# Optimization experiments

Hardware: AMD Instinct MI355X
Metric: run time of the kernel (lower is better)

Reference implementation:

```python
import math
import jax, jax.numpy as jnp
import numpy as np

B, S, D = 2, 2048, 1024
H = 16
R = 256
NC = 16
NE = 16
NK = 4096
KR = 256
TOPK = 8


def setup_inputs() -> dict:
    key = jax.random.key(0)
    ks = jax.random.split(key, 16)
    n = lambda k, shape, s: jax.random.normal(k, shape, jnp.float32) * s
    d = {}
    d['x'] = jax.random.normal(ks[0], (B, S, D), jnp.float32)
    d['importance'] = jax.random.uniform(ks[1], (B, S), jnp.float32)
    # global router weights (nn.Linear(d_model, n, bias=False) -> [n, d_model])
    d['Wc'] = n(ks[2], (NC, D), 0.02)
    d['WQ'] = n(ks[3], (NE, D), 0.02)
    d['WK'] = n(ks[4], (NE, D), 0.02)
    d['WV'] = n(ks[5], (NE, D), 0.02)
    d['Wm'] = n(ks[6], (NC, D), 0.02)
    # shared neuron pools (orthogonal init approximated by scaled gaussian)
    d['compress_neurons'] = n(ks[7], (NC, D, R), 1.0 / math.sqrt(D))
    d['expand_pool'] = n(ks[8], (NE, R, D), 1.0 / math.sqrt(R))
    d['knowledge_K'] = n(ks[9], (NK, KR), 0.02)
    d['knowledge_V'] = n(ks[10], (NK, D), 0.02)
    d['W_O'] = n(ks[11], (D, D), 1.0 / math.sqrt(D))
    d['g1'] = jnp.ones((D,), jnp.float32)
    d['b1'] = jnp.zeros((D,), jnp.float32)
    d['g2'] = jnp.ones((D,), jnp.float32)
    d['b2'] = jnp.zeros((D,), jnp.float32)
    return d


def _ln(x, g, b):
    mu = x.mean(-1, keepdims=True)
    v = ((x - mu) ** 2).mean(-1, keepdims=True)
    return (x - mu) * jax.lax.rsqrt(v + 1e-5) * g + b


def _route(nx, imp, W):
    # softmax over expert axis, importance-weighted pool over sequence, renormalize
    pref = jax.nn.softmax(nx @ W.T, axis=-1)          # [B,S,n]
    w = jnp.einsum('bs,bsn->bn', imp, pref)
    return w / (w.sum(-1, keepdims=True) + 1e-8)


def reference(x, importance, Wc, WQ, WK, WV, Wm, compress_neurons, expand_pool,
              knowledge_K, knowledge_V, W_O, g1, b1, g2, b2):
    Bx, Sx, Dm = x.shape
    dh = Dm // H
    # --- attention sub-block ---
    nx = _ln(x, g1, b1)
    cw = _route(nx, importance, Wc)
    qw = _route(nx, importance, WQ)
    kw = _route(nx, importance, WK)
    vw = _route(nx, importance, WV)
    sc = jnp.einsum('bn,ndr->bdr', cw, compress_neurons)   # per-batch compress [B,D,R]
    h = jnp.einsum('bsd,bdr->bsr', nx, sc)                 # [B,S,R]

    def expand(w):
        e = jnp.einsum('bn,nrd->brd', w, expand_pool)      # [B,R,D]
        return jnp.einsum('bsr,brd->bsd', h, e)            # [B,S,D]

    Q = expand(qw).reshape(Bx, Sx, H, dh).transpose(0, 2, 1, 3)
    K = expand(kw).reshape(Bx, Sx, H, dh).transpose(0, 2, 1, 3)
    V = expand(vw).reshape(Bx, Sx, H, dh).transpose(0, 2, 1, 3)
    scores = jnp.einsum('bhqd,bhkd->bhqk', Q, K) / math.sqrt(dh)
    causal = jnp.tril(jnp.ones((Sx, Sx), bool))
    scores = jnp.where(causal, scores, -jnp.inf)
    attn = jax.nn.softmax(scores, axis=-1)
    ao = jnp.einsum('bhqk,bhkd->bhqd', attn, V)
    ao = ao.transpose(0, 2, 1, 3).reshape(Bx, Sx, Dm)
    x = x + ao @ W_O.T
    # --- memory sub-block ---
    nx2 = _ln(x, g2, b2)
    mw = _route(nx2, importance, Wm)
    mc = jnp.einsum('bn,ndr->bdr', mw, compress_neurons)
    Qm = jnp.einsum('bsd,bdr->bsr', nx2, mc)              # [B,S,R]
    ms = Qm @ knowledge_K.T / math.sqrt(KR)               # [B,S,NK]
    tv, ti = jax.lax.top_k(ms, TOPK)                      # [B,S,k]
    w = jax.nn.softmax(tv, axis=-1)
    mem = jnp.einsum('bsk,bskd->bsd', w, knowledge_V[ti])
    return x + mem
```

## Files before the change

kernel.cpp:

```cpp
#include <hip/hip_runtime.h>
#include <hip/hip_bf16.h>
#include <math.h>

typedef __bf16 bf16;
typedef __attribute__((ext_vector_type(8))) __bf16 bf16x8;
typedef __attribute__((ext_vector_type(4))) __bf16 bf16x4;
typedef __attribute__((ext_vector_type(4))) float f32x4;
typedef __attribute__((ext_vector_type(16))) float f32x16;

#define EXP2N __builtin_amdgcn_exp2f

static __device__ __forceinline__ void gload_lds16(const bf16* g, bf16* l) {
  __builtin_amdgcn_global_load_lds((const __attribute__((address_space(1))) void*)g,
                                   (__attribute__((address_space(3))) void*)l, 16, 0, 0);
}

__global__ __launch_bounds__(256) void ln_kernel(
    const float* __restrict__ x, const float* __restrict__ gam, const float* __restrict__ bet,
    bf16* __restrict__ nxo)
{
  const int token = blockIdx.x;
  const int t = threadIdx.x, w = t >> 6, l = t & 63;
  __shared__ float red1[4], red2[4];
  float4 xv = ((const float4*)(x + (size_t)token * 1024))[t];
  float s  = xv.x + xv.y + xv.z + xv.w;
  float sq = xv.x*xv.x + xv.y*xv.y + xv.z*xv.z + xv.w*xv.w;
  #pragma unroll
  for (int off = 32; off > 0; off >>= 1) { s += __shfl_xor(s, off); sq += __shfl_xor(sq, off); }
  if (l == 0) { red1[w] = s; red2[w] = sq; }
  __syncthreads();
  s  = red1[0] + red1[1] + red1[2] + red1[3];
  sq = red2[0] + red2[1] + red2[2] + red2[3];
  const float mu  = s * (1.f / 1024.f);
  const float var = sq * (1.f / 1024.f) - mu * mu;
  const float rs  = rsqrtf(var + 1e-5f);
  float4 gv = ((const float4*)gam)[t];
  float4 bv = ((const float4*)bet)[t];
  bf16x4 pk = {(bf16)((xv.x - mu) * rs * gv.x + bv.x),
               (bf16)((xv.y - mu) * rs * gv.y + bv.y),
               (bf16)((xv.z - mu) * rs * gv.z + bv.z),
               (bf16)((xv.w - mu) * rs * gv.w + bv.w)};
  *(bf16x4*)(nxo + (size_t)token * 1024 + t * 4) = pk;
}

__global__ __launch_bounds__(256) void route_pool_kernel(
    const float* __restrict__ logits, const float* __restrict__ imp,
    float* __restrict__ racc, int ng, int gbase)
{
  const int w = threadIdx.x >> 6, l = threadIdx.x & 63;
  const int token = blockIdx.x * 4 + w;
  const int b = token >> 11;
  const int g = l >> 4, e = l & 15;
  if (g < ng) {
    float v = logits[(size_t)token * 128 + g * 16 + e];
    float mx = v;
    #pragma unroll
    for (int off = 1; off < 16; off <<= 1) mx = fmaxf(mx, __shfl_xor(mx, off));
    float ex = __expf(v - mx);
    float sm = ex;
    #pragma unroll
    for (int off = 1; off < 16; off <<= 1) sm += __shfl_xor(sm, off);
    atomicAdd(racc + ((((size_t)(token & 31)) * 5 + gbase + g) * 2 + b) * 16 + e,
              imp[token] * (ex / sm));
  }
}

__global__ __launch_bounds__(256) void mixA_kernel(
    const float* __restrict__ comp, const float* __restrict__ expd,
    const float* __restrict__ racc, bf16* __restrict__ sct, bf16* __restrict__ eqt)
{
  const int xb = blockIdx.x, sel = blockIdx.y, b = blockIdx.z;
  const int t = threadIdx.x;
  __shared__ float tile[64][65];
  __shared__ float psh[3][16];
  __shared__ float dsh[3];
  if (sel == 0) {
    if (t < 16) {
      float s = 0.f;
      for (int sl = 0; sl < 32; ++sl) s += racc[(((size_t)sl * 5 + 0) * 2 + b) * 16 + t];
      psh[0][t] = s;
    }
  } else {
    if (t < 48) {
      const int g = t >> 4, e = t & 15;
      float s = 0.f;
      for (int sl = 0; sl < 32; ++sl) s += racc[(((size_t)sl * 5 + 1 + g) * 2 + b) * 16 + e];
      psh[g][e] = s;
    }
  }
  __syncthreads();
  if (t < ((sel == 0) ? 1 : 3)) {
    float den = 1e-8f;
    #pragma unroll
    for (int e = 0; e < 16; ++e) den += psh[t][e];
    dsh[t] = 1.0f / den;
  }
  __syncthreads();

  const int ri = t >> 2, cc = (t & 3) << 4;
  if (sel == 0) {
    const int i0 = (xb & 15) * 64, j0 = (xb >> 4) * 64;
    const float inv = dsh[0];
    float acc[16];
    #pragma unroll
    for (int k = 0; k < 16; ++k) acc[k] = 0.f;
    const float* src0 = comp + ((size_t)(i0 + ri)) * 256 + j0 + cc;
    #pragma unroll 4
    for (int n = 0; n < 16; ++n) {
      const float wv = psh[0][n] * inv;
      const float4* sp = (const float4*)(src0 + (size_t)n * 262144);
      #pragma unroll
      for (int q = 0; q < 4; ++q) {
        float4 v = sp[q];
        acc[q*4+0] += wv * v.x; acc[q*4+1] += wv * v.y;
        acc[q*4+2] += wv * v.z; acc[q*4+3] += wv * v.w;
      }
    }
    #pragma unroll
    for (int k = 0; k < 16; ++k) tile[ri][cc + k] = acc[k];
    __syncthreads();
    union { bf16 h[16]; bf16x8 v[2]; } ob;
    #pragma unroll
    for (int k = 0; k < 16; ++k) ob.h[k] = (bf16)tile[cc + k][ri];
    bf16* dst = sct + ((size_t)b * 256 + j0 + ri) * 1024 + i0 + cc;
    ((bf16x8*)dst)[0] = ob.v[0];
    ((bf16x8*)dst)[1] = ob.v[1];
  } else {
    const int i0 = (xb & 3) * 64, j0 = (xb >> 2) * 64;
    const float inv0 = dsh[0], inv1 = dsh[1], inv2 = dsh[2];
    float acc[3][16];
    #pragma unroll
    for (int g = 0; g < 3; ++g)
      #pragma unroll
      for (int k = 0; k < 16; ++k) acc[g][k] = 0.f;
    const float* src0 = expd + ((size_t)(i0 + ri)) * 1024 + j0 + cc;
    #pragma unroll 2
    for (int n = 0; n < 16; ++n) {
      const float w0 = psh[0][n] * inv0;
      const float w1 = psh[1][n] * inv1;
      const float w2 = psh[2][n] * inv2;
      const float4* sp = (const float4*)(src0 + (size_t)n * 262144);
      #pragma unroll
      for (int q = 0; q < 4; ++q) {
        float4 v = sp[q];
        acc[0][q*4+0] += w0 * v.x; acc[0][q*4+1] += w0 * v.y;
        acc[0][q*4+2] += w0 * v.z; acc[0][q*4+3] += w0 * v.w;
        acc[1][q*4+0] += w1 * v.x; acc[1][q*4+1] += w1 * v.y;
        acc[1][q*4+2] += w1 * v.z; acc[1][q*4+3] += w1 * v.w;
        acc[2][q*4+0] += w2 * v.x; acc[2][q*4+1] += w2 * v.y;
        acc[2][q*4+2] += w2 * v.z; acc[2][q*4+3] += w2 * v.w;
      }
    }
    #pragma unroll 1
    for (int g = 0; g < 3; ++g) {
      __syncthreads();
      #pragma unroll
      for (int k = 0; k < 16; ++k) tile[ri][cc + k] = acc[g][k];
      __syncthreads();
      union { bf16 h[16]; bf16x8 v[2]; } ob;
      #pragma unroll
      for (int k = 0; k < 16; ++k) ob.h[k] = (bf16)tile[cc + k][ri];
      bf16* dst = eqt + (size_t)g * 524288 + ((size_t)b * 1024 + j0 + ri) * 256 + i0 + cc;
      ((bf16x8*)dst)[0] = ob.v[0];
      ((bf16x8*)dst)[1] = ob.v[1];
    }
  }
}

__global__ __launch_bounds__(256) void mixB_kernel(
    const float* __restrict__ comp, const float* __restrict__ racc,
    bf16* __restrict__ out)
{
  const int xb = blockIdx.x, b = blockIdx.z;
  const int t = threadIdx.x;
  __shared__ float tile[64][65];
  __shared__ float psh[16];
  __shared__ float dsh1;
  if (t < 16) {
    float s = 0.f;
    for (int sl = 0; sl < 32; ++sl) s += racc[(((size_t)sl * 5 + 4) * 2 + b) * 16 + t];
    psh[t] = s;
  }
  __syncthreads();
  if (t == 0) {
    float den = 1e-8f;
    #pragma unroll
    for (int e = 0; e < 16; ++e) den += psh[e];
    dsh1 = 1.0f / den;
  }
  __syncthreads();
  const int ri = t >> 2, cc = (t & 3) << 4;
  const int i0 = (xb & 15) * 64, j0 = (xb >> 4) * 64;
  const float inv = dsh1;
  float acc[16];
  #pragma unroll
  for (int k = 0; k < 16; ++k) acc[k] = 0.f;
  const float* src0 = comp + ((size_t)(i0 + ri)) * 256 + j0 + cc;
  #pragma unroll 4
  for (int n = 0; n < 16; ++n) {
    const float wv = psh[n] * inv;
    const float4* sp = (const float4*)(src0 + (size_t)n * 262144);
    #pragma unroll
    for (int q = 0; q < 4; ++q) {
      float4 v = sp[q];
      acc[q*4+0] += wv * v.x; acc[q*4+1] += wv * v.y;
      acc[q*4+2] += wv * v.z; acc[q*4+3] += wv * v.w;
    }
  }
  #pragma unroll
  for (int k = 0; k < 16; ++k) tile[ri][cc + k] = acc[k];
  __syncthreads();
  union { bf16 h[16]; bf16x8 v[2]; } ob;
  #pragma unroll
  for (int k = 0; k < 16; ++k) ob.h[k] = (bf16)tile[cc + k][ri];
  bf16* dst = out + ((size_t)b * 256 + j0 + ri) * 1024 + i0 + cc;
  ((bf16x8*)dst)[0] = ob.v[0];
  ((bf16x8*)dst)[1] = ob.v[1];
}

__global__ void cvt_bf16_kernel(const float* __restrict__ in, bf16* __restrict__ out, int n4)
{
  const int i = blockIdx.x * 256 + threadIdx.x;
  if (i < n4) {
    float4 v = ((const float4*)in)[i];
    bf16x4 o = {(bf16)v.x, (bf16)v.y, (bf16)v.z, (bf16)v.w};
    ((bf16x4*)out)[i] = o;
  }
}

__global__ void cvt_all_kernel(
    const float* __restrict__ w0, const float* __restrict__ w1,
    const float* __restrict__ w2, const float* __restrict__ w3,
    const float* __restrict__ w4, bf16* __restrict__ wcat,
    const float* __restrict__ wo, bf16* __restrict__ woo,
    const float* __restrict__ kk, bf16* __restrict__ kko)
{
  int i = blockIdx.x * 256 + threadIdx.x;
  if (i < 32768) {
    const int seg = i >> 12;
    bf16x4 o;
    if (seg < 5) {
      const float* src = (seg == 0) ? w0 : (seg == 1) ? w1 : (seg == 2) ? w2
                       : (seg == 3) ? w3 : w4;
      float4 v = ((const float4*)src)[i & 4095];
      o = (bf16x4){(bf16)v.x, (bf16)v.y, (bf16)v.z, (bf16)v.w};
    } else {
      o = (bf16x4){(bf16)0.f, (bf16)0.f, (bf16)0.f, (bf16)0.f};
    }
    ((bf16x4*)wcat)[i] = o;
  } else {
    i -= 32768;
    if (i < 262144) {
      float4 v = ((const float4*)wo)[i];
      ((bf16x4*)woo)[i] = (bf16x4){(bf16)v.x, (bf16)v.y, (bf16)v.z, (bf16)v.w};
    } else {
      i -= 262144;
      float4 v = ((const float4*)kk)[i];
      ((bf16x4*)kko)[i] = (bf16x4){(bf16)v.x, (bf16)v.y, (bf16)v.z, (bf16)v.w};
    }
  }
}

template<int CMODE>
__global__ __launch_bounds__(512) void gemm_bt(
    const bf16* __restrict__ A, const bf16* __restrict__ Bt, void* __restrict__ Cp,
    const float* __restrict__ resid, int M, int N, int K, int lda, int ldb,
    long sA, long sB, long sC, float scale)
{
  __shared__ alignas(16) bf16 As[128 * 32];
  __shared__ alignas(16) bf16 Bs[128 * 32];
  const int t = threadIdx.x, w = t >> 6, l = t & 63;
  const int llo = l & 15, lhi = l >> 4;
  const int wm = w >> 2, wn = w & 3;
  const int m0 = blockIdx.y * 128, n0 = blockIdx.x * 128;
  const int z = blockIdx.z;
  const bf16* Ab;
  const bf16* Bb;
  if (CMODE == 5) {
    Ab = A  + (size_t)(z >> 1) * sA + (size_t)(z & 1) * K;
    Bb = Bt + (size_t)(z >> 1) * sB + (size_t)(z & 1) * K;
  } else if (CMODE == 6) {
    Ab = A  + (size_t)(z & 1) * sA;
    Bb = Bt + (size_t)(z >> 1) * 524288 + (size_t)(z & 1) * sB;
  } else {
    Ab = A  + (size_t)z * sA;
    Bb = Bt + (size_t)z * sB;
  }
  f32x4 acc[4][2];
  #pragma unroll
  for (int i = 0; i < 4; ++i)
    #pragma unroll
    for (int j = 0; j < 2; ++j) acc[i][j] = (f32x4){0.f, 0.f, 0.f, 0.f};

  const int arow = t >> 2, akb = t & 3;
  const bf16* asrc = Ab + (size_t)(m0 + arow) * lda + akb * 8;
  const bf16* bsrc = Bb + (size_t)(n0 + arow) * ldb + akb * 8;
  const int aoff0 = arow * 64 + ((akb * 16) ^ (((arow >> 1) & 3) << 4));

  uint4 a0 = *(const uint4*)(asrc);
  uint4 b0 = *(const uint4*)(bsrc);

  for (int kt = 0; kt < K; kt += 32) {
    __syncthreads();
    *(uint4*)((char*)As + aoff0) = a0;
    *(uint4*)((char*)Bs + aoff0) = b0;
    __syncthreads();
    if (kt + 32 < K) {
      a0 = *(const uint4*)(asrc + kt + 32);
      b0 = *(const uint4*)(bsrc + kt + 32);
    }
    bf16x8 af[4], bfr[2];
    #pragma unroll
    for (int fi = 0; fi < 4; ++fi) {
      int r = wm * 64 + fi * 16 + llo;
      af[fi] = *(const bf16x8*)((const char*)As + (r * 64 + ((lhi * 16) ^ (((r >> 1) & 3) << 4))));
    }
    #pragma unroll
    for (int fj = 0; fj < 2; ++fj) {
      int c = wn * 32 + fj * 16 + llo;
      bfr[fj] = *(const bf16x8*)((const char*)Bs + (c * 64 + ((lhi * 16) ^ (((c >> 1) & 3) << 4))));
    }
    #pragma unroll
    for (int fi = 0; fi < 4; ++fi)
      #pragma unroll
      for (int fj = 0; fj < 2; ++fj)
        acc[fi][fj] = __builtin_amdgcn_mfma_f32_16x16x32_bf16(af[fi], bfr[fj], acc[fi][fj], 0, 0, 0);
  }

  size_t cbase;
  if (CMODE == 4) cbase = 0;
  else if (CMODE == 5) cbase = (size_t)(z >> 1) * sC;
  else if (CMODE == 6) cbase = (size_t)(z & 1) * sC;
  else cbase = (size_t)z * sC;

  #pragma unroll
  for (int fi = 0; fi < 4; ++fi)
    #pragma unroll
    for (int fj = 0; fj < 2; ++fj)
      #pragma unroll
      for (int jj = 0; jj < 4; ++jj) {
        int r = m0 + wm * 64 + fi * 16 + lhi * 4 + jj;
        int c = n0 + wn * 32 + fj * 16 + llo;
        size_t idx = cbase + (size_t)r * N + c;
        float v = acc[fi][fj][jj] * ((CMODE == 6) ? 1.0f : scale);
        if (CMODE == 0) {
          ((bf16*)Cp)[idx] = (bf16)v;
        } else if (CMODE == 3) {
          size_t idx3 = (((size_t)z * 16 + (c >> 6)) * 2048 + r) * 64 + (c & 63);
          ((bf16*)Cp)[idx3] = (bf16)v;
        } else if (CMODE == 4 || CMODE == 5) {
          atomicAdd(&((float*)Cp)[idx], v);
        } else if (CMODE == 6) {
          if ((z >> 1) == 0) {
            ((bf16*)Cp)[idx] = (bf16)v;
          } else {
            size_t idx3 = (((size_t)(z & 1) * 16 + (c >> 6)) * 2048 + r) * 64 + (c & 63);
            ((bf16*)resid)[idx3] = (bf16)(v * scale);
          }
        } else {
          if (CMODE == 2) v += resid[idx];
          ((float*)Cp)[idx] = v;
        }
      }
}

static __device__ __forceinline__ unsigned pk2f(float a, float b) {
  union { bf16 h[2]; unsigned u; } x;
  x.h[0] = (bf16)a; x.h[1] = (bf16)b; return x.u;
}

__global__ __launch_bounds__(512, 2) void attn7_kernel(
    const bf16* __restrict__ Qg, const bf16* __restrict__ Khg,
    const bf16* __restrict__ Vtg, bf16* __restrict__ aog)
{
  __shared__ alignas(16) bf16 KS[2][2][4096];
  __shared__ alignas(16) bf16 VS[2][2][4096];
  const int lin = blockIdx.x;
  const int hb = lin & 31, jj = (lin >> 5) & 7, phase = lin >> 8;
  const int h = hb >> 1, b = hb & 1;
  const int t = threadIdx.x, w = t >> 6, l = t & 63;
  const int half = w >> 2, wsub = w & 3;
  const int qi = l & 31, hi = l >> 5;
  const bf16* Qb = Qg  + ((size_t)b * 2048) * 1024 + h * 64;
  const bf16* Kh = Khg + ((size_t)(b * 16 + h)) * 2048 * 64;
  const bf16* Vh = Vtg + ((size_t)b * 1024 + h * 64) * 2048;
  bf16* Ob = aog + ((size_t)b * 2048) * 1024 + h * 64;

  float* PO = (float*)&KS[0][0][0];
  float* MM = (float*)((char*)&KS[0][0][0] + 40960);
  float* LL = MM + 128;

  auto ISSUE = [&](int bi, int kv0) {
    bf16* ksb = &KS[half][bi][0];
    bf16* vsb = &VS[half][bi][0];
    #pragma unroll
    for (int i = 0; i < 2; ++i) {
      int c = wsub * 128 + i * 64 + l;
      int row = c >> 3;
      int scol = (c & 7) ^ (row & 7);
      gload_lds16(Kh + (size_t)(kv0 + row) * 64 + scol * 8,
                  (bf16*)((char*)ksb + wsub * 2048 + i * 1024));
    }
    #pragma unroll
    for (int i = 0; i < 2; ++i) {
      int c = wsub * 128 + i * 64 + l;
      int row = c >> 3;
      int scol = (c & 7) ^ (row & 7);
      gload_lds16(Vh + (size_t)row * 2048 + kv0 + scol * 8,
                  (bf16*)((char*)vsb + wsub * 2048 + i * 1024));
    }
  };

  const int T = phase ? (15 - jj) : jj;
  const int q0 = T * 128 + wsub * 32;
  const int base_g = half * (T + 1);

  bf16x8 qf[4];
  #pragma unroll
  for (int dc = 0; dc < 4; ++dc)
    qf[dc] = *(const bf16x8*)(Qb + (size_t)(q0 + qi) * 1024 + dc * 16 + hi * 8);

  f32x16 o0, o1;
  #pragma unroll
  for (int r = 0; r < 16; ++r) { o0[r] = 0.f; o1[r] = 0.f; }
  float m_run = -INFINITY, l_run = 0.f;

  ISSUE(0, base_g * 64);

  auto STEP64 = [&](int bi, int s0) {
    const bool h2 = (s0 + 32 <= q0);
    bf16x8 kf[8];
    const bf16* ksb = &KS[half][bi][0];
    const bf16* vsb = &VS[half][bi][0];
    const int kr1 = qi, kr2 = 32 + qi;
    #pragma unroll
    for (int dc = 0; dc < 4; ++dc) {
      kf[dc]     = *(const bf16x8*)((const char*)ksb + kr1 * 128 +
                                    (((dc * 2 + hi) ^ (kr1 & 7)) << 4));
      kf[4 + dc] = *(const bf16x8*)((const char*)ksb + kr2 * 128 +
                                    (((dc * 2 + hi) ^ (kr2 & 7)) << 4));
    }
    f32x16 sv1, sv2;
    #pragma unroll
    for (int r = 0; r < 16; ++r) { sv1[r] = 0.f; sv2[r] = 0.f; }
    __builtin_amdgcn_s_setprio(1);
    #pragma unroll
    for (int dc = 0; dc < 4; ++dc)
      sv1 = __builtin_amdgcn_mfma_f32_32x32x16_bf16(kf[dc], qf[dc], sv1, 0, 0, 0);
    if (h2) {
      #pragma unroll
      for (int dc = 0; dc < 4; ++dc)
        sv2 = __builtin_amdgcn_mfma_f32_32x32x16_bf16(kf[4 + dc], qf[dc], sv2, 0, 0, 0);
    }
    __builtin_amdgcn_s_setprio(0);
    const int qe = qi - 4 * hi;
    if (s0 == q0) {
      #pragma unroll
      for (int r = 0; r < 16; ++r) {
        const int kvc = (r & 3) + 8 * (r >> 2);
        sv1[r] = (kvc > qe) ? -INFINITY : sv1[r];
      }
    }
    if (h2 && s0 + 32 == q0) {
      #pragma unroll
      for (int r = 0; r < 16; ++r) {
        const int kvc = (r & 3) + 8 * (r >> 2);
        sv2[r] = (kvc > qe) ? -INFINITY : sv2[r];
      }
    }
    float mx[8];
    #pragma unroll
    for (int i = 0; i < 8; ++i) mx[i] = fmaxf(sv1[2 * i], sv1[2 * i + 1]);
    if (h2) {
      #pragma unroll
      for (int i = 0; i < 8; ++i) mx[i] = fmaxf(mx[i], fmaxf(sv2[2 * i], sv2[2 * i + 1]));
    }
    #pragma unroll
    for (int i = 0; i < 4; ++i) mx[i] = fmaxf(mx[i], mx[i + 4]);
    float tm = fmaxf(fmaxf(mx[0], mx[1]), fmaxf(mx[2], mx[3]));
    tm = fmaxf(tm, __shfl_xor(tm, 32));
    if (!__all(tm <= m_run + 11.0f)) {
      const float mn = fmaxf(m_run, tm);
      const float alpha = EXP2N(m_run - mn);
      m_run = mn;
      l_run *= alpha;
      o0 *= alpha; o1 *= alpha;
    }
    float rs = 0.f;
    unsigned pk[16], ot[16];
    #pragma unroll
    for (int i = 0; i < 8; ++i) {
      float pa = EXP2N(sv1[2 * i]     - m_run);
      float pb = EXP2N(sv1[2 * i + 1] - m_run);
      rs += pa + pb;
      pk[i] = pk2f(pa, pb);
    }
    if (h2) {
      #pragma unroll
      for (int i = 0; i < 8; ++i) {
        float pa = EXP2N(sv2[2 * i]     - m_run);
        float pb = EXP2N(sv2[2 * i + 1] - m_run);
        rs += pa + pb;
        pk[8 + i] = pk2f(pa, pb);
      }
    }
    rs += __shfl_xor(rs, 32);
    l_run += rs;
    #pragma unroll
    for (int i = 0; i < 8; ++i) ot[i] = __shfl_xor(pk[i], 32);
    if (h2) {
      #pragma unroll
      for (int i = 0; i < 8; ++i) ot[8 + i] = __shfl_xor(pk[8 + i], 32);
    }
    __builtin_amdgcn_s_setprio(1);
    #pragma unroll
    for (int c2 = 0; c2 < 4; ++c2) {
      if (c2 < 2 || h2) {
        union { unsigned u[4]; bf16x8 v; } pf;
        pf.u[0] = hi ? ot[4 * c2 + 2] : pk[4 * c2 + 0];
        pf.u[1] = hi ? ot[4 * c2 + 3] : pk[4 * c2 + 1];
        pf.u[2] = hi ? pk[4 * c2 + 2] : ot[4 * c2 + 0];
        pf.u[3] = hi ? pk[4 * c2 + 3] : ot[4 * c2 + 1];
        const int d0 = qi, d1 = 32 + qi;
        bf16x8 v0 = *(const bf16x8*)((const char*)vsb + d0 * 128 +
                                     (((c2 * 2 + hi) ^ (d0 & 7)) << 4));
        bf16x8 v1 = *(const bf16x8*)((const char*)vsb + d1 * 128 +
                                     (((c2 * 2 + hi) ^ (d1 & 7)) << 4));
        o0 = __builtin_amdgcn_mfma_f32_32x32x16_bf16(v0, pf.v, o0, 0, 0, 0);
        o1 = __builtin_amdgcn_mfma_f32_32x32x16_bf16(v1, pf.v, o1, 0, 0, 0);
      }
    }
    __builtin_amdgcn_s_setprio(0);
  };

  #pragma unroll 1
  for (int st = 0; st <= T; ++st) {
    const int bi = st & 1;
    if (st < T) {
      ISSUE(bi ^ 1, (base_g + st + 1) * 64);
      asm volatile("s_waitcnt vmcnt(4)" ::: "memory");
    } else {
      asm volatile("s_waitcnt vmcnt(0)" ::: "memory");
    }
    __builtin_amdgcn_s_barrier();
    const int s0 = (base_g + st) * 64;
    if (s0 <= q0) STEP64(bi, s0);
    __builtin_amdgcn_s_barrier();
  }

  if (half == 1) {
    #pragma unroll
    for (int r = 0; r < 16; ++r) {
      const int d0 = (r & 3) + 8 * (r >> 2) + 4 * hi;
      PO[(wsub * 32 + qi) * 65 + d0]      = o0[r];
      PO[(wsub * 32 + qi) * 65 + 32 + d0] = o1[r];
    }
    if (hi == 0) { MM[wsub * 32 + qi] = m_run; LL[wsub * 32 + qi] = l_run; }
  }
  __syncthreads();
  if (half == 0) {
    const float m1 = MM[wsub * 32 + qi], l1 = LL[wsub * 32 + qi];
    const float m = fmaxf(m_run, m1);
    const float a0 = EXP2N(m_run - m), a1 = EXP2N(m1 - m);
    const float inv = 1.0f / (a0 * l_run + a1 * l1);
    #pragma unroll
    for (int rg = 0; rg < 4; ++rg) {
      union { bf16 h4[4]; unsigned long long u; } pr0, pr1;
      #pragma unroll
      for (int e = 0; e < 4; ++e) {
        const int r = rg * 4 + e;
        const int d0 = (r & 3) + 8 * (r >> 2) + 4 * hi;
        pr0.h4[e] = (bf16)((a0 * o0[r] + a1 * PO[(wsub * 32 + qi) * 65 + d0])      * inv);
        pr1.h4[e] = (bf16)((a0 * o1[r] + a1 * PO[(wsub * 32 + qi) * 65 + 32 + d0]) * inv);
      }
      *(unsigned long long*)(Ob + (size_t)(q0 + qi) * 1024 +  0 + rg * 8 + hi * 4) = pr0.u;
      *(unsigned long long*)(Ob + (size_t)(q0 + qi) * 1024 + 32 + rg * 8 + hi * 4) = pr1.u;
    }
  }
}

static __device__ __forceinline__ void ce_desc(float& a, float& b) {
  float hi = fmaxf(a, b), lo = fminf(a, b); a = hi; b = lo;
}
static __device__ __forceinline__ void merge8(float r[8], const float o[8]) {
  float c[8];
  #pragma unroll
  for (int i = 0; i < 8; ++i) c[i] = fmaxf(r[i], o[7 - i]);
  ce_desc(c[0], c[4]); ce_desc(c[1], c[5]); ce_desc(c[2], c[6]); ce_desc(c[3], c[7]);
  ce_desc(c[0], c[2]); ce_desc(c[1], c[3]); ce_desc(c[4], c[6]); ce_desc(c[5], c[7]);
  ce_desc(c[0], c[1]); ce_desc(c[2], c[3]); ce_desc(c[4], c[5]); ce_desc(c[6], c[7]);
  #pragma unroll
  for (int i = 0; i < 8; ++i) r[i] = c[i];
}
static __device__ __forceinline__ unsigned long long fkey(float v, int idx) {
  unsigned u = __float_as_uint(v);
  u = (u & 0x80000000u) ? ~u : (u | 0x80000000u);
  return ((unsigned long long)u << 32) | (unsigned)(0xFFFFFFFFu - (unsigned)idx);
}

__global__ __launch_bounds__(256) void topk3_kernel(
    const bf16* __restrict__ ms, const float* __restrict__ kV, float* __restrict__ outp)
{
  const int token = blockIdx.x;
  const int t = threadIdx.x, w = t >> 6, l = t & 63;
  __shared__ unsigned long long cand[4096];
  __shared__ float wmax[32];
  __shared__ float wv[8];
  __shared__ int   wi[8];
  __shared__ int   cnt;
  if (t == 0) cnt = 0;

  const bf16* mrow = ms + (size_t)token * 4096;
  float vv[16];
  #pragma unroll
  for (int c = 0; c < 2; ++c) {
    bf16x8 rv = ((const bf16x8*)mrow)[t + c * 256];
    #pragma unroll
    for (int j = 0; j < 8; ++j) vv[c * 8 + j] = (float)rv[j];
  }

  float m = vv[0];
  #pragma unroll
  for (int j = 1; j < 16; ++j) m = fmaxf(m, vv[j]);

  float r[8];
  r[0] = m;
  #pragma unroll
  for (int i = 1; i < 8; ++i) r[i] = -INFINITY;
  #pragma unroll
  for (int st = 0; st < 6; ++st) {
    const int off = 1 << st;
    float o[8];
    #pragma unroll
    for (int i = 0; i < 8; ++i) o[i] = __shfl_xor(r[i], off);
    merge8(r, o);
  }
  if (l == 0) {
    #pragma unroll
    for (int i = 0; i < 8; ++i) wmax[w * 8 + i] = r[i];
  }
  __syncthreads();

  float a[8], bb[8];
  #pragma unroll
  for (int i = 0; i < 8; ++i) { a[i] = wmax[i]; bb[i] = wmax[8 + i]; }
  merge8(a, bb);
  #pragma unroll
  for (int i = 0; i < 8; ++i) bb[i] = wmax[16 + i];
  {
    float c2[8];
    #pragma unroll
    for (int i = 0; i < 8; ++i) c2[i] = wmax[24 + i];
    merge8(bb, c2);
  }
  merge8(a, bb);
  const float t8 = a[7];

  #pragma unroll
  for (int c = 0; c < 2; ++c) {
    const int base = (t + c * 256) * 8;
    #pragma unroll
    for (int j = 0; j < 8; ++j) {
      float v = vv[c * 8 + j];
      if (v >= t8) { int pos = atomicAdd(&cnt, 1); cand[pos] = fkey(v, base + j); }
    }
  }
  __syncthreads();

  if (w == 0) {
    const int n = cnt;
    unsigned long long prev = ~0ULL;
    float vk[8]; int ik[8];
    #pragma unroll
    for (int k = 0; k < 8; ++k) {
      unsigned long long best = 0;
      for (int i = l; i < n; i += 64) {
        unsigned long long c = cand[i];
        if (c < prev && c > best) best = c;
      }
      #pragma unroll
      for (int st = 0; st < 6; ++st) {
        const int off = 1 << st;
        unsigned bh = (unsigned)(best >> 32), bl = (unsigned)best;
        unsigned oh = __shfl_xor(bh, off), ol = __shfl_xor(bl, off);
        unsigned long long ob = ((unsigned long long)oh << 32) | ol;
        if (ob > best) best = ob;
      }
      prev = best;
      unsigned u = (unsigned)(best >> 32);
      u = (u & 0x80000000u) ? (u ^ 0x80000000u) : ~u;
      vk[k] = __uint_as_float(u);
      ik[k] = (int)(0xFFFFFFFFu - (unsigned)(best & 0xFFFFFFFFu));
    }
    if (l == 0) {
      const float mx = vk[0];
      float den = 0.f, ex[8];
      #pragma unroll
      for (int k = 0; k < 8; ++k) { ex[k] = __expf(vk[k] - mx); den += ex[k]; }
      const float inv = 1.0f / den;
      #pragma unroll
      for (int k = 0; k < 8; ++k) { wv[k] = ex[k] * inv; wi[k] = ik[k]; }
    }
  }
  __syncthreads();

  float a0 = 0, a1 = 0, a2 = 0, a3 = 0;
  #pragma unroll
  for (int k = 0; k < 8; ++k) {
    const float wk = wv[k];
    float4 vr = *(const float4*)(kV + (size_t)wi[k] * 1024 + t * 4);
    a0 += wk * vr.x; a1 += wk * vr.y; a2 += wk * vr.z; a3 += wk * vr.w;
  }
  float4* op = (float4*)(outp + (size_t)token * 1024) + t;
  float4 cur = *op;
  cur.x += a0; cur.y += a1; cur.z += a2; cur.w += a3;
  *op = cur;
}

extern "C" void kernel_launch(void* const* d_in, const int* in_sizes, int n_in,
                              void* d_out, int out_size, void* d_ws, size_t ws_size,
                              hipStream_t stream)
{
  (void)in_sizes; (void)n_in; (void)out_size; (void)ws_size;
  const float* x    = (const float*)d_in[0];
  const float* imp  = (const float*)d_in[1];
  const float* Wc   = (const float*)d_in[2];
  const float* WQ   = (const float*)d_in[3];
  const float* WK   = (const float*)d_in[4];
  const float* WV   = (const float*)d_in[5];
  const float* Wm   = (const float*)d_in[6];
  const float* comp = (const float*)d_in[7];
  const float* expd = (const float*)d_in[8];
  const float* kK   = (const float*)d_in[9];
  const float* kV   = (const float*)d_in[10];
  const float* WO   = (const float*)d_in[11];
  const float* g1   = (const float*)d_in[12];
  const float* b1   = (const float*)d_in[13];
  const float* g2   = (const float*)d_in[14];
  const float* b2   = (const float*)d_in[15];
  float* out = (float*)d_out;
  char* ws = (char*)d_ws;
  const size_t MB = 1u << 20;
  float* racc    = (float*)(ws);
  float* logits1 = (float*)(ws + 64 * 1024);
  float* logits2 = (float*)(ws + 64 * 1024 + 2 * MB);
  float* accf1   = (float*)(ws + 64 * 1024 + 4 * MB);
  float* accf2   = (float*)(ws + 64 * 1024 + 8 * MB);
  bf16*  Wcatb   = (bf16*)(ws + 13 * MB);
  char* ar = ws + 14 * MB;
  bf16* nx   = (bf16*)(ar);
  bf16* sct  = (bf16*)(ar +  8 * MB);
  bf16* eqt  = (bf16*)(ar +  9 * MB);
  bf16* evt  = (bf16*)(ar + 11 * MB);
  bf16* hb   = (bf16*)(ar + 12 * MB);
  bf16* Qb   = (bf16*)(ar + 14 * MB);
  bf16* Kb   = (bf16*)(ar + 22 * MB);
  bf16* Vtb  = (bf16*)(ar + 30 * MB);
  bf16* aob  = (bf16*)(ar + 38 * MB);
  bf16* WOb  = (bf16*)(ar + 46 * MB);
  bf16* nx2  = (bf16*)(ar);
  bf16* mct  = (bf16*)(ar +  8 * MB);
  bf16* Qmb  = (bf16*)(ar +  9 * MB);
  bf16* kKb  = (bf16*)(ar + 11 * MB);
  bf16* msb  = (bf16*)(ar + 13 * MB);

  hipMemsetAsync(ws, 0, 12 * MB + 65536, stream);
  cvt_all_kernel<<<2176, 256, 0, stream>>>(Wc, WQ, WK, WV, Wm, Wcatb, WO, WOb, kK, kKb);

  ln_kernel<<<4096, 256, 0, stream>>>(x, g1, b1, nx);
  gemm_bt<4><<<dim3(1, 32, 4), 512, 0, stream>>>(nx, Wcatb, logits1, nullptr,
        4096, 128, 256, 1024, 1024, 256L, 256L, 0L, 1.0f);
  route_pool_kernel<<<1024, 256, 0, stream>>>(logits1, imp, racc, 4, 0);
  mixA_kernel<<<dim3(64, 2, 2), 256, 0, stream>>>(comp, expd, racc, sct, eqt);
  gemm_bt<5><<<dim3(2, 16, 4), 512, 0, stream>>>(nx, sct, accf1, nullptr, 2048, 256, 512,
        1024, 1024, (long)2048 * 1024, (long)256 * 1024, (long)2048 * 256, 1.0f);
  cvt_bf16_kernel<<<1024, 256, 0, stream>>>(accf1, hb, 262144);
  gemm_bt<6><<<dim3(8, 16, 4), 512, 0, stream>>>(hb, eqt, Qb, (const float*)Kb,
        2048, 1024, 256, 256, 256,
        (long)2048 * 256, (long)1024 * 256, (long)2048 * 1024, 0.18033688f);
  gemm_bt<0><<<dim3(16, 8, 2), 512, 0, stream>>>(evt, hb, Vtb, nullptr, 1024, 2048, 256,
        256, 256, (long)1024 * 256, (long)2048 * 256, (long)1024 * 2048, 1.0f);
  attn7_kernel<<<512, 512, 0, stream>>>(Qb, Kb, Vtb, aob);
  gemm_bt<2><<<dim3(8, 32, 1), 512, 0, stream>>>(aob, WOb, out, x, 4096, 1024, 1024,
        1024, 1024, 0L, 0L, 0L, 1.0f);
  ln_kernel<<<4096, 256, 0, stream>>>(out, g2, b2, nx2);
  gemm_bt<4><<<dim3(1, 32, 4), 512, 0, stream>>>(nx2, Wcatb + 64 * 1024, logits2, nullptr,
        4096, 128, 256, 1024, 1024, 256L, 256L, 0L, 1.0f);
  route_pool_kernel<<<1024, 256, 0, stream>>>(logits2, imp, racc, 1, 4);
  mixB_kernel<<<dim3(64, 1, 2), 256, 0, stream>>>(comp, racc, mct);
  gemm_bt<5><<<dim3(2, 16, 4), 512, 0, stream>>>(nx2, mct, accf2, nullptr, 2048, 256, 512,
        1024, 1024, (long)2048 * 1024, (long)256 * 1024, (long)2048 * 256, 1.0f);
  cvt_bf16_kernel<<<1024, 256, 0, stream>>>(accf2, Qmb, 262144);
  gemm_bt<0><<<dim3(32, 16, 2), 512, 0, stream>>>(Qmb, kKb, msb, nullptr, 2048, 4096, 256,
        256, 256, (long)2048 * 256, 0L, (long)2048 * 4096, 0.0625f);
  topk3_kernel<<<4096, 256, 0, stream>>>(msb, kV, out);
}
```

Measured before the change: 249.6 us.

## Double-buffer gemm_bt tiles using direct global-to-LDS async loads

```diff
diff --git a/kernel.cpp b/kernel.cpp
--- a/kernel.cpp
+++ b/kernel.cpp
@@ -267,8 +267,8 @@
     const float* __restrict__ resid, int M, int N, int K, int lda, int ldb,
     long sA, long sB, long sC, float scale)
 {
-  __shared__ alignas(16) bf16 As[128 * 32];
-  __shared__ alignas(16) bf16 Bs[128 * 32];
+  __shared__ alignas(16) bf16 As[2][128 * 32];
+  __shared__ alignas(16) bf16 Bs[2][128 * 32];
   const int t = threadIdx.x, w = t >> 6, l = t & 63;
   const int llo = l & 15, lhi = l >> 4;
   const int wm = w >> 2, wn = w & 3;
@@ -293,38 +293,43 @@
     for (int j = 0; j < 2; ++j) acc[i][j] = (f32x4){0.f, 0.f, 0.f, 0.f};
 
   const int arow = t >> 2, akb = t & 3;
-  const bf16* asrc = Ab + (size_t)(m0 + arow) * lda + akb * 8;
-  const bf16* bsrc = Bb + (size_t)(n0 + arow) * ldb + akb * 8;
-  const int aoff0 = arow * 64 + ((akb * 16) ^ (((arow >> 1) & 3) << 4));
-
-  uint4 a0 = *(const uint4*)(asrc);
-  uint4 b0 = *(const uint4*)(bsrc);
-
+  const int akbs = akb ^ ((arow >> 1) & 3);
+  const bf16* asrc = Ab + (size_t)(m0 + arow) * lda + akbs * 8;
+  const bf16* bsrc = Bb + (size_t)(n0 + arow) * ldb + akbs * 8;
+  bf16* adst0 = &As[0][t * 8];
+  bf16* bdst0 = &Bs[0][t * 8];
+  bf16* adst1 = &As[1][t * 8];
+  bf16* bdst1 = &Bs[1][t * 8];
+
+  gload_lds16(asrc, adst0);
+  gload_lds16(bsrc, bdst0);
+
+  int buf = 0;
   for (int kt = 0; kt < K; kt += 32) {
     __syncthreads();
-    *(uint4*)((char*)As + aoff0) = a0;
-    *(uint4*)((char*)Bs + aoff0) = b0;
-    __syncthreads();
     if (kt + 32 < K) {
-      a0 = *(const uint4*)(asrc + kt + 32);
-      b0 = *(const uint4*)(bsrc + kt + 32);
-    }
+      gload_lds16(asrc + kt + 32, buf ? adst0 : adst1);
+      gload_lds16(bsrc + kt + 32, buf ? bdst0 : bdst1);
+    }
+    const bf16* Asb = As[buf];
+    const bf16* Bsb = Bs[buf];
     bf16x8 af[4], bfr[2];
     #pragma unroll
     for (int fi = 0; fi < 4; ++fi) {
       int r = wm * 64 + fi * 16 + llo;
-      af[fi] = *(const bf16x8*)((const char*)As + (r * 64 + ((lhi * 16) ^ (((r >> 1) & 3) << 4))));
+      af[fi] = *(const bf16x8*)((const char*)Asb + (r * 64 + ((lhi * 16) ^ (((r >> 1) & 3) << 4))));
     }
     #pragma unroll
     for (int fj = 0; fj < 2; ++fj) {
       int c = wn * 32 + fj * 16 + llo;
-      bfr[fj] = *(const bf16x8*)((const char*)Bs + (c * 64 + ((lhi * 16) ^ (((c >> 1) & 3) << 4))));
+      bfr[fj] = *(const bf16x8*)((const char*)Bsb + (c * 64 + ((lhi * 16) ^ (((c >> 1) & 3) << 4))));
     }
     #pragma unroll
     for (int fi = 0; fi < 4; ++fi)
       #pragma unroll
       for (int fj = 0; fj < 2; ++fj)
         acc[fi][fj] = __builtin_amdgcn_mfma_f32_16x16x32_bf16(af[fi], bfr[fj], acc[fi][fj], 0, 0, 0);
+    buf ^= 1;
   }
 
   size_t cbase;
```

Result: faster. 244.3 us (-2.1%).
